# Kernel tuning notes

Measured on AMD Instinct MI355X. Metric: run time of the kernel, lower is better.

The kernel has to match this reference:

```python
import jax, jax.numpy as jnp
import numpy as np


def setup_inputs() -> dict:
    key = jax.random.key(0)
    k1, k2, k3, k4 = jax.random.split(key, 4)
    batch, d_in, d_out, K, M = 4096, 1024, 1024, 16, 512
    x = jax.random.normal(k1, (batch, d_in), dtype=jnp.float32)
    A = jax.random.normal(k2, (K, d_in, M), dtype=jnp.float32) * (1.0 / np.sqrt(d_in))
    B = jax.random.normal(k3, (K, M, d_out), dtype=jnp.float32) * (1.0 / np.sqrt(M))
    bias = jnp.zeros((d_out,), dtype=jnp.float32)
    topk_mask = jax.random.randint(k4, (batch, K), 0, 2) > 0
    return {"x": x, "topk_mask": topk_mask, "A": A, "B": B, "bias": bias}


def reference(x, topk_mask, A, B, bias):
    # pre_inner_acts: [batch, k, m]
    pre = jnp.einsum('bi,kim->bkm', x, A)
    maskf = topk_mask.astype(pre.dtype)[:, :, None]  # [batch, k, 1]
    pre = pre * maskf
    # inner_acts: [batch, k, out]
    inner_acts = jnp.einsum('bkm,kmh->bkh', pre, B)
    inner_acts = inner_acts * maskf
    out = jnp.sum(inner_acts, axis=1) + bias  # [batch, out]
    return out, inner_acts
```

## Files before the change

### kernel.cpp

```cpp
#include <hip/hip_runtime.h>

typedef __attribute__((ext_vector_type(8))) short bf16x8;
typedef __attribute__((ext_vector_type(4))) float f32x4;

__device__ __forceinline__ unsigned short f2bf(float f) {
  union { float f; unsigned u; } v; v.f = f;
  unsigned r = v.u + 0x7fffu + ((v.u >> 16) & 1u);
  return (unsigned short)(r >> 16);
}

__global__ __launch_bounds__(256)
void prep_kernel(const float* __restrict__ x, unsigned short* __restrict__ x_bf,
                 const float* __restrict__ A, unsigned short* __restrict__ A_t,
                 const int* __restrict__ mask, int* __restrict__ rows,
                 int* __restrict__ counts) {
  __shared__ float tbuf[32][33];
  __shared__ int cnt, mcnt;
  const int bid = blockIdx.x;
  const int t = threadIdx.x;

  if (bid < 4096) {
    int i = bid * 256 + t;
    float4 v = ((const float4*)x)[i];
    ushort4 o; o.x = f2bf(v.x); o.y = f2bf(v.y); o.z = f2bf(v.z); o.w = f2bf(v.w);
    ((ushort4*)x_bf)[i] = o;
    return;
  }
  if (bid < 12288) {
    int local = (bid - 4096) & 511;
    int z = (bid - 4096) >> 9;
    const int R = 1024, C = 512;
    int cx = local & 15, ry = local >> 4;
    size_t eo = (size_t)z * R * C;
    const float* src = A + eo;
    unsigned short* dst = A_t + eo;
    int c0 = cx * 32, r0 = ry * 32;
    int tx = t & 31, ty = t >> 5;
#pragma unroll
    for (int i = 0; i < 32; i += 8)
      tbuf[ty + i][tx] = src[(size_t)(r0 + ty + i) * C + (c0 + tx)];
    __syncthreads();
#pragma unroll
    for (int i = 0; i < 32; i += 8)
      dst[(size_t)(c0 + ty + i) * R + (r0 + tx)] = f2bf(tbuf[tx][ty + i]);
    return;
  }
  {
    int z = bid - 12288;
    if (t == 0) { cnt = 0; mcnt = 0; }
    __syncthreads();
    int* rz = rows + (size_t)z * 4096;
    for (int i = t; i < 4096; i += 256) {
      bool m = mask[(size_t)i * 16 + z] != 0;
      unsigned long long bal = __ballot(m);
      int lane = t & 63;
      int pa = __popcll(bal & ((1ull << lane) - 1ull));
      int ta = __popcll(bal);
      int base_a, base_m;
      if (lane == 0) { base_a = atomicAdd(&cnt, ta); base_m = atomicAdd(&mcnt, 64 - ta); }
      base_a = __shfl(base_a, 0);
      base_m = __shfl(base_m, 0);
      int pm = lane - pa;
      if (m) rz[base_a + pa] = i;
      else   rz[4095 - (base_m + pm)] = i;
    }
    __syncthreads();
    if (t == 0) counts[z] = cnt;
  }
}

__device__ __forceinline__ void stage_tile(const unsigned short* __restrict__ src,
                                           size_t row_stride, int row0, int k0,
                                           unsigned short* lds) {
  int t = threadIdx.x;
  int lane = t & 63;
  int w = t >> 6;
#pragma unroll
  for (int i = 0; i < 4; ++i) {
    int chunk = w * 4 + i;
    int row = chunk * 8 + (lane >> 3);
    int glog = (lane & 7) ^ (row & 7);
    const unsigned short* g = src + (size_t)(row0 + row) * row_stride + (size_t)(k0 + glog * 8);
    __builtin_amdgcn_global_load_lds((const __attribute__((address_space(1))) unsigned int*)g,
                                     (__attribute__((address_space(3))) unsigned int*)(lds + chunk * 512),
                                     16, 0, 0);
  }
}

__device__ __forceinline__ void stage_tile_gather(const unsigned short* __restrict__ src,
                                                  const int* __restrict__ rowsS, int k0,
                                                  unsigned short* lds) {
  int t = threadIdx.x;
  int lane = t & 63;
  int w = t >> 6;
#pragma unroll
  for (int i = 0; i < 4; ++i) {
    int chunk = w * 4 + i;
    int row = chunk * 8 + (lane >> 3);
    int glog = (lane & 7) ^ (row & 7);
    const unsigned short* g = src + (size_t)rowsS[row] * 1024 + (size_t)(k0 + glog * 8);
    __builtin_amdgcn_global_load_lds((const __attribute__((address_space(1))) unsigned int*)g,
                                     (__attribute__((address_space(3))) unsigned int*)(lds + chunk * 512),
                                     16, 0, 0);
  }
}

__device__ __forceinline__ bf16x8 read_frag(const unsigned short* lds, int row, int gb) {
  int phys = (row * 128 + gb) ^ ((row & 7) << 4);
  return *(const bf16x8*)((const char*)lds + phys);
}

__global__ __launch_bounds__(256)
void gemm1_fused_kernel(const unsigned short* __restrict__ X,
                        const unsigned short* __restrict__ W,
                        unsigned short* __restrict__ pre_out,
                        const float* __restrict__ B, unsigned short* __restrict__ B_t,
                        const int* __restrict__ rows,
                        const int* __restrict__ counts) {
  __shared__ unsigned short Xs[128 * 64];
  __shared__ unsigned short Ws[128 * 64];
  __shared__ int rowsS[128];
  __shared__ float tbuf[32][33];

  const int o = blockIdx.x;
  const int chunk = o & 7;
  const int pos = o >> 3;
  const int t = threadIdx.x;

  if (pos >= 256) {
    int tr = chunk * 1024 + (pos - 256);
    int z = tr >> 9;
    int local = tr & 511;
    const int R = 512, C = 1024;
    int cx = local & 31, ry = local >> 5;
    size_t eo = (size_t)z * R * C;
    const float* src = B + eo;
    unsigned short* dst = B_t + eo;
    int c0 = cx * 32, r0 = ry * 32;
    int tx = t & 31, ty = t >> 5;
#pragma unroll
    for (int i = 0; i < 32; i += 8)
      tbuf[ty + i][tx] = src[(size_t)(r0 + ty + i) * C + (c0 + tx)];
    __syncthreads();
#pragma unroll
    for (int i = 0; i < 32; i += 8)
      dst[(size_t)(c0 + ty + i) * R + (r0 + tx)] = f2bf(tbuf[tx][ty + i]);
    return;
  }

  int g = chunk * 256 + pos;
  const int bx = g & 3;
  const int by = (g >> 2) & 31;
  const int z = g >> 7;

  const int cnt = counts[z];
  const int tb = by * 128;
  const int tn = bx * 128;
  if (tb >= cnt) return;

  if (t < 128) rowsS[t] = rows[(size_t)z * 4096 + tb + t];
  __syncthreads();

  const int lane = t & 63;
  const int wv = t >> 6;
  const int wr = (wv >> 1) * 64;
  const int wc = (wv & 1) * 64;
  const int fr = lane & 15;
  const int fg = lane >> 4;

  const unsigned short* Wbase = W + (size_t)z * 512 * 1024;

  f32x4 acc[4][4] = {};

  for (int kt = 0; kt < 16; ++kt) {
    if (kt) __syncthreads();
    stage_tile_gather(X, rowsS, kt * 64, Xs);
    stage_tile(Wbase, 1024, tn, kt * 64, Ws);
    __syncthreads();
#pragma unroll
    for (int kk = 0; kk < 2; ++kk) {
      const int gb = kk * 64 + fg * 16;
      bf16x8 xf[4], wf[4];
#pragma unroll
      for (int i = 0; i < 4; ++i) {
        xf[i] = read_frag(Xs, wr + i * 16 + fr, gb);
        wf[i] = read_frag(Ws, wc + i * 16 + fr, gb);
      }
#pragma unroll
      for (int mi = 0; mi < 4; ++mi)
#pragma unroll
        for (int ni = 0; ni < 4; ++ni)
          acc[mi][ni] = __builtin_amdgcn_mfma_f32_16x16x32_bf16(xf[mi], wf[ni], acc[mi][ni], 0, 0, 0);
    }
  }

#pragma unroll
  for (int mi = 0; mi < 4; ++mi) {
#pragma unroll
    for (int j = 0; j < 4; ++j) {
      int rl = wr + mi * 16 + fg * 4 + j;
      size_t rowbase = (size_t)z * 4096 * 512 + (size_t)(tb + rl) * 512;
#pragma unroll
      for (int ni = 0; ni < 4; ++ni) {
        int m = tn + wc + ni * 16 + fr;
        pre_out[rowbase + m] = f2bf(acc[mi][ni][j]);
      }
    }
  }
}

__global__ __launch_bounds__(256)
void gemm2_kernel(const unsigned short* __restrict__ X,
                  const unsigned short* __restrict__ W,
                  float* __restrict__ inner_out,
                  const int* __restrict__ rows,
                  const int* __restrict__ counts) {
  const int gx = gridDim.x, gy = gridDim.y;
  int lin = blockIdx.x + gx * (blockIdx.y + gy * blockIdx.z);
  int cpx = (gx * gy * gridDim.z) >> 3;
  lin = (lin & 7) * cpx + (lin >> 3);
  int bx = lin % gx; lin /= gx;
  int by = lin % gy; lin /= gy;
  const int z = lin;
  const int cnt = counts[z];
  const int tb = by * 128;
  const int tn = bx * 128;
  const int t = threadIdx.x;

  __shared__ unsigned short Xs[128 * 64];
  __shared__ unsigned short Ws[128 * 64];
  __shared__ int rowsS[128];

  if (t < 128) rowsS[t] = rows[(size_t)z * 4096 + tb + t];
  __syncthreads();

  if (tb >= cnt) {
    const float4 z4 = {0.f, 0.f, 0.f, 0.f};
#pragma unroll
    for (int it = 0; it < 16; ++it) {
      int rl = it * 8 + (t >> 5);
      int b = rowsS[rl];
      ((float4*)(inner_out + (size_t)b * (16 * 1024) + (size_t)z * 1024 + tn))[t & 31] = z4;
    }
    return;
  }

  const int lane = t & 63;
  const int wv = t >> 6;
  const int wr = (wv >> 1) * 64;
  const int wc = (wv & 1) * 64;
  const int fr = lane & 15;
  const int fg = lane >> 4;

  const unsigned short* Xbase = X + (size_t)z * 4096 * 512;
  const unsigned short* Wbase = W + (size_t)z * 1024 * 512;

  f32x4 acc[4][4] = {};

  for (int kt = 0; kt < 8; ++kt) {
    if (kt) __syncthreads();
    stage_tile(Xbase, 512, tb, kt * 64, Xs);
    stage_tile(Wbase, 512, tn, kt * 64, Ws);
    __syncthreads();
#pragma unroll
    for (int kk = 0; kk < 2; ++kk) {
      const int gb = kk * 64 + fg * 16;
      bf16x8 xf[4], wf[4];
#pragma unroll
      for (int i = 0; i < 4; ++i) {
        xf[i] = read_frag(Xs, wr + i * 16 + fr, gb);
        wf[i] = read_frag(Ws, wc + i * 16 + fr, gb);
      }
#pragma unroll
      for (int mi = 0; mi < 4; ++mi)
#pragma unroll
        for (int ni = 0; ni < 4; ++ni)
          acc[mi][ni] = __builtin_amdgcn_mfma_f32_16x16x32_bf16(xf[mi], wf[ni], acc[mi][ni], 0, 0, 0);
    }
  }

#pragma unroll
  for (int mi = 0; mi < 4; ++mi) {
#pragma unroll
    for (int j = 0; j < 4; ++j) {
      int rl = wr + mi * 16 + fg * 4 + j;
      int b = rowsS[rl];
      size_t rowbase = (size_t)b * (16 * 1024) + (size_t)z * 1024;
      if (tb + rl < cnt) {
#pragma unroll
        for (int ni = 0; ni < 4; ++ni) {
          int h = tn + wc + ni * 16 + fr;
          inner_out[rowbase + h] = acc[mi][ni][j];
        }
      } else {
#pragma unroll
        for (int ni = 0; ni < 4; ++ni) {
          int h = tn + wc + ni * 16 + fr;
          inner_out[rowbase + h] = 0.f;
        }
      }
    }
  }
}

__global__ __launch_bounds__(256)
void reduce_kernel(const float* __restrict__ inner, const float* __restrict__ bias,
                   const int* __restrict__ mask, float* __restrict__ out) {
  int b = blockIdx.x;
  int t = threadIdx.x;
  __shared__ int mrow[16];
  if (t < 16) mrow[t] = mask[(size_t)b * 16 + t];
  __syncthreads();
  float4 s = ((const float4*)bias)[t];
  const float4* ip = (const float4*)(inner + (size_t)b * (16 * 1024)) + t;
#pragma unroll
  for (int k = 0; k < 16; ++k) {
    if (mrow[k]) {
      float4 v = ip[(size_t)k * 256];
      s.x += v.x; s.y += v.y; s.z += v.z; s.w += v.w;
    }
  }
  ((float4*)out)[(size_t)b * 256 + t] = s;
}

extern "C" void kernel_launch(void* const* d_in, const int* in_sizes, int n_in,
                              void* d_out, int out_size, void* d_ws, size_t ws_size,
                              hipStream_t stream) {
  const float* x    = (const float*)d_in[0];
  const int*   mask = (const int*)d_in[1];
  const float* A    = (const float*)d_in[2];
  const float* B    = (const float*)d_in[3];
  const float* bias = (const float*)d_in[4];

  float* out   = (float*)d_out;
  float* inner = (float*)d_out + (size_t)4096 * 1024;

  if (ws_size < 109314112ull) return;
  char* ws = (char*)d_ws;
  unsigned short* x_bf = (unsigned short*)ws;
  unsigned short* A_t  = (unsigned short*)(ws + ((size_t)8 << 20));
  unsigned short* B_t  = (unsigned short*)(ws + ((size_t)24 << 20));
  unsigned short* pre  = (unsigned short*)(ws + ((size_t)40 << 20));
  int* rows            = (int*)(ws + ((size_t)104 << 20));
  int* counts          = (int*)(ws + ((size_t)104 << 20) + 262144);

  prep_kernel<<<12304, 256, 0, stream>>>(x, x_bf, A, A_t, mask, rows, counts);

  gemm1_fused_kernel<<<10240, 256, 0, stream>>>(x_bf, A_t, pre, B, B_t, rows, counts);
  gemm2_kernel<<<dim3(8, 32, 16), 256, 0, stream>>>(pre, B_t, inner, rows, counts);

  reduce_kernel<<<4096, 256, 0, stream>>>(inner, bias, mask, out);
}
```

Baseline: 194.1 us.

## Move B transpose into prep kernel, widen transpose tiles, precompute gather offsets

Moves the B fp32-to-bf16 transpose out of the GEMM1 launch and into the prep kernel, using 64x64 transpose tiles and 8-wide bf16 conversion stores for x. GEMM1 becomes a plain 3D-grid kernel with XCD-aware block remapping, and its gathered X row offsets are computed once instead of every k-step. GEMM2 writes its zero outputs with nontemporal stores. The aims are fewer blocks, less address arithmetic and less cache pollution, though the B conversion no longer overlaps with GEMM1 compute.

```diff
diff --git a/kernel.cpp b/kernel.cpp
--- a/kernel.cpp
+++ b/kernel.cpp
@@ -2,6 +2,7 @@
 
 typedef __attribute__((ext_vector_type(8))) short bf16x8;
 typedef __attribute__((ext_vector_type(4))) float f32x4;
+typedef __attribute__((ext_vector_type(8))) unsigned short u16x8;
 
 __device__ __forceinline__ unsigned short f2bf(float f) {
   union { float f; unsigned u; } v; v.f = f;
@@ -12,41 +13,51 @@
 __global__ __launch_bounds__(256)
 void prep_kernel(const float* __restrict__ x, unsigned short* __restrict__ x_bf,
                  const float* __restrict__ A, unsigned short* __restrict__ A_t,
+                 const float* __restrict__ B, unsigned short* __restrict__ B_t,
                  const int* __restrict__ mask, int* __restrict__ rows,
                  int* __restrict__ counts) {
-  __shared__ float tbuf[32][33];
+  __shared__ float tbuf[64][65];
   __shared__ int cnt, mcnt;
   const int bid = blockIdx.x;
   const int t = threadIdx.x;
 
-  if (bid < 4096) {
-    int i = bid * 256 + t;
-    float4 v = ((const float4*)x)[i];
-    ushort4 o; o.x = f2bf(v.x); o.y = f2bf(v.y); o.z = f2bf(v.z); o.w = f2bf(v.w);
-    ((ushort4*)x_bf)[i] = o;
+  if (bid < 2048) {
+    int slot = bid * 256 + t;
+    float4 v0 = ((const float4*)x)[2 * slot];
+    float4 v1 = ((const float4*)x)[2 * slot + 1];
+    u16x8 o;
+    o[0] = f2bf(v0.x); o[1] = f2bf(v0.y); o[2] = f2bf(v0.z); o[3] = f2bf(v0.w);
+    o[4] = f2bf(v1.x); o[5] = f2bf(v1.y); o[6] = f2bf(v1.z); o[7] = f2bf(v1.w);
+    ((u16x8*)x_bf)[slot] = o;
     return;
   }
-  if (bid < 12288) {
-    int local = (bid - 4096) & 511;
-    int z = (bid - 4096) >> 9;
-    const int R = 1024, C = 512;
-    int cx = local & 15, ry = local >> 4;
+  if (bid < 6144) {
+    const float* in; unsigned short* out; int R, C, cx, ry, z;
+    if (bid < 4096) {
+      int idx = bid - 2048; z = idx >> 7; int local = idx & 127;
+      R = 1024; C = 512; cx = local & 7; ry = local >> 3;
+      in = A; out = A_t;
+    } else {
+      int idx = bid - 4096; z = idx >> 7; int local = idx & 127;
+      R = 512; C = 1024; cx = local & 15; ry = local >> 4;
+      in = B; out = B_t;
+    }
     size_t eo = (size_t)z * R * C;
-    const float* src = A + eo;
-    unsigned short* dst = A_t + eo;
-    int c0 = cx * 32, r0 = ry * 32;
-    int tx = t & 31, ty = t >> 5;
-#pragma unroll
-    for (int i = 0; i < 32; i += 8)
+    const float* src = in + eo;
+    unsigned short* dst = out + eo;
+    int c0 = cx * 64, r0 = ry * 64;
+    int tx = t & 63, ty = t >> 6;
+#pragma unroll
+    for (int i = 0; i < 64; i += 4)
       tbuf[ty + i][tx] = src[(size_t)(r0 + ty + i) * C + (c0 + tx)];
     __syncthreads();
 #pragma unroll
-    for (int i = 0; i < 32; i += 8)
+    for (int i = 0; i < 64; i += 4)
       dst[(size_t)(c0 + ty + i) * R + (r0 + tx)] = f2bf(tbuf[tx][ty + i]);
     return;
   }
   {
-    int z = bid - 12288;
+    int z = bid - 6144;
     if (t == 0) { cnt = 0; mcnt = 0; }
     __syncthreads();
     int* rz = rows + (size_t)z * 4096;
@@ -87,76 +98,34 @@
   }
 }
 
-__device__ __forceinline__ void stage_tile_gather(const unsigned short* __restrict__ src,
-                                                  const int* __restrict__ rowsS, int k0,
-                                                  unsigned short* lds) {
-  int t = threadIdx.x;
-  int lane = t & 63;
-  int w = t >> 6;
-#pragma unroll
-  for (int i = 0; i < 4; ++i) {
-    int chunk = w * 4 + i;
-    int row = chunk * 8 + (lane >> 3);
-    int glog = (lane & 7) ^ (row & 7);
-    const unsigned short* g = src + (size_t)rowsS[row] * 1024 + (size_t)(k0 + glog * 8);
-    __builtin_amdgcn_global_load_lds((const __attribute__((address_space(1))) unsigned int*)g,
-                                     (__attribute__((address_space(3))) unsigned int*)(lds + chunk * 512),
-                                     16, 0, 0);
-  }
-}
-
 __device__ __forceinline__ bf16x8 read_frag(const unsigned short* lds, int row, int gb) {
   int phys = (row * 128 + gb) ^ ((row & 7) << 4);
   return *(const bf16x8*)((const char*)lds + phys);
 }
 
 __global__ __launch_bounds__(256)
-void gemm1_fused_kernel(const unsigned short* __restrict__ X,
-                        const unsigned short* __restrict__ W,
-                        unsigned short* __restrict__ pre_out,
-                        const float* __restrict__ B, unsigned short* __restrict__ B_t,
-                        const int* __restrict__ rows,
-                        const int* __restrict__ counts) {
+void gemm1_kernel(const unsigned short* __restrict__ X,
+                  const unsigned short* __restrict__ W,
+                  unsigned short* __restrict__ pre_out,
+                  const int* __restrict__ rows,
+                  const int* __restrict__ counts) {
+  const int gx = gridDim.x, gy = gridDim.y;
+  int lin = blockIdx.x + gx * (blockIdx.y + gy * blockIdx.z);
+  int cpx = (gx * gy * gridDim.z) >> 3;
+  lin = (lin & 7) * cpx + (lin >> 3);
+  int bx = lin % gx; lin /= gx;
+  int by = lin % gy; lin /= gy;
+  const int z = lin;
+  const int cnt = counts[z];
+  const int tb = by * 128;
+  const int tn = bx * 128;
+  const int t = threadIdx.x;
+
+  if (tb >= cnt) return;
+
   __shared__ unsigned short Xs[128 * 64];
   __shared__ unsigned short Ws[128 * 64];
   __shared__ int rowsS[128];
-  __shared__ float tbuf[32][33];
-
-  const int o = blockIdx.x;
-  const int chunk = o & 7;
-  const int pos = o >> 3;
-  const int t = threadIdx.x;
-
-  if (pos >= 256) {
-    int tr = chunk * 1024 + (pos - 256);
-    int z = tr >> 9;
-    int local = tr & 511;
-    const int R = 512, C = 1024;
-    int cx = local & 31, ry = local >> 5;
-    size_t eo = (size_t)z * R * C;
-    const float* src = B + eo;
-    unsigned short* dst = B_t + eo;
-    int c0 = cx * 32, r0 = ry * 32;
-    int tx = t & 31, ty = t >> 5;
-#pragma unroll
-    for (int i = 0; i < 32; i += 8)
-      tbuf[ty + i][tx] = src[(size_t)(r0 + ty + i) * C + (c0 + tx)];
-    __syncthreads();
-#pragma unroll
-    for (int i = 0; i < 32; i += 8)
-      dst[(size_t)(c0 + ty + i) * R + (r0 + tx)] = f2bf(tbuf[tx][ty + i]);
-    return;
-  }
-
-  int g = chunk * 256 + pos;
-  const int bx = g & 3;
-  const int by = (g >> 2) & 31;
-  const int z = g >> 7;
-
-  const int cnt = counts[z];
-  const int tb = by * 128;
-  const int tn = bx * 128;
-  if (tb >= cnt) return;
 
   if (t < 128) rowsS[t] = rows[(size_t)z * 4096 + tb + t];
   __syncthreads();
@@ -170,11 +139,29 @@
 
   const unsigned short* Wbase = W + (size_t)z * 512 * 1024;
 
+  int xoff[4];
+#pragma unroll
+  for (int i = 0; i < 4; ++i) {
+    int chunk = wv * 4 + i;
+    int row = chunk * 8 + (lane >> 3);
+    int glog = (lane & 7) ^ (row & 7);
+    xoff[i] = rowsS[row] * 1024 + glog * 8;
+  }
+
   f32x4 acc[4][4] = {};
 
   for (int kt = 0; kt < 16; ++kt) {
     if (kt) __syncthreads();
-    stage_tile_gather(X, rowsS, kt * 64, Xs);
+    {
+      const int k64 = kt * 64;
+#pragma unroll
+      for (int i = 0; i < 4; ++i) {
+        int chunk = wv * 4 + i;
+        __builtin_amdgcn_global_load_lds(
+            (const __attribute__((address_space(1))) unsigned int*)(X + xoff[i] + k64),
+            (__attribute__((address_space(3))) unsigned int*)(Xs + chunk * 512), 16, 0, 0);
+      }
+    }
     stage_tile(Wbase, 1024, tn, kt * 64, Ws);
     __syncthreads();
 #pragma unroll
@@ -235,12 +222,13 @@
   __syncthreads();
 
   if (tb >= cnt) {
-    const float4 z4 = {0.f, 0.f, 0.f, 0.f};
+    const f32x4 z4 = {0.f, 0.f, 0.f, 0.f};
 #pragma unroll
     for (int it = 0; it < 16; ++it) {
       int rl = it * 8 + (t >> 5);
       int b = rowsS[rl];
-      ((float4*)(inner_out + (size_t)b * (16 * 1024) + (size_t)z * 1024 + tn))[t & 31] = z4;
+      f32x4* p = (f32x4*)(inner_out + (size_t)b * (16 * 1024) + (size_t)z * 1024 + tn) + (t & 31);
+      __builtin_nontemporal_store(z4, p);
     }
     return;
   }
@@ -296,7 +284,7 @@
 #pragma unroll
         for (int ni = 0; ni < 4; ++ni) {
           int h = tn + wc + ni * 16 + fr;
-          inner_out[rowbase + h] = 0.f;
+          __builtin_nontemporal_store(0.f, &inner_out[rowbase + h]);
         }
       }
     }
@@ -344,9 +332,9 @@
   int* rows            = (int*)(ws + ((size_t)104 << 20));
   int* counts          = (int*)(ws + ((size_t)104 << 20) + 262144);
 
-  prep_kernel<<<12304, 256, 0, stream>>>(x, x_bf, A, A_t, mask, rows, counts);
-
-  gemm1_fused_kernel<<<10240, 256, 0, stream>>>(x_bf, A_t, pre, B, B_t, rows, counts);
+  prep_kernel<<<6160, 256, 0, stream>>>(x, x_bf, A, A_t, B, B_t, mask, rows, counts);
+
+  gemm1_kernel<<<dim3(4, 32, 16), 256, 0, stream>>>(x_bf, A_t, pre, rows, counts);
   gemm2_kernel<<<dim3(8, 32, 16), 256, 0, stream>>>(pre, B_t, inner, rows, counts);
 
   reduce_kernel<<<4096, 256, 0, stream>>>(inner, bias, mask, out);
```

Measured after the change: 166.8 us. -14.1%, faster.
